# Kernel tuning notes

Hardware: AMD Instinct MI355X
Metric: run time of the kernel (lower is better)

## Reference

```python
import jax, jax.numpy as jnp
import numpy as np

IN_FEATURES = 4096
OUT_FEATURES = 11008


def setup_inputs() -> dict:
    key = jax.random.key(0)
    k1, k2, k3 = jax.random.split(key, 3)
    x = jax.random.normal(k1, (4, 2048, IN_FEATURES), dtype=jnp.float32)
    # int8-valued weights stored as int32 (range [-127, 127] emulated via [0,127) here)
    weight_quantized = jax.random.randint(k2, (OUT_FEATURES, IN_FEATURES), 0, 127, dtype=jnp.int32)
    weight_scale = jax.random.uniform(k3, (OUT_FEATURES,), dtype=jnp.float32) * 0.01 + 1e-4
    return {"x": x, "weight_quantized": weight_quantized, "weight_scale": weight_scale}


def reference(x, weight_quantized, weight_scale):
    # Dequantize: per-output-channel scale, then dense GEMM (F.linear semantics: y = x @ W^T)
    weight_fp = weight_quantized.astype(x.dtype) * weight_scale[:, None].astype(x.dtype)
    # x: [B, S, in], weight_fp: [out, in] -> [B, S, out]
    return jnp.einsum('bsi,oi->bso', x, weight_fp)
```

## Files before the change

### kernel.cpp

```cpp
#include <hip/hip_runtime.h>
#include <stdint.h>
#include <stddef.h>

#define M_DIM 8192
#define N_DIM 11008
#define K_DIM 4096

typedef __attribute__((ext_vector_type(8))) __bf16 bf16x8;
typedef __attribute__((ext_vector_type(4))) float f32x4;

typedef const __attribute__((address_space(1))) void gvoid;
typedef __attribute__((address_space(3))) void lvoid;

__device__ __forceinline__ void async16(const void* g, void* l) {
  __builtin_amdgcn_global_load_lds((gvoid*)g, (lvoid*)l, 16, 0, 0);
}

__device__ __forceinline__ unsigned short f2bf(float f) {
  unsigned u = __float_as_uint(f);
  u += 0x7fffu + ((u >> 16) & 1u);
  return (unsigned short)(u >> 16);
}


__global__ __launch_bounds__(256) void cvt_x_kernel(const float* __restrict__ x,
                                                    unsigned short* __restrict__ xw) {
  size_t i = ((size_t)blockIdx.x * 256 + threadIdx.x) * 4;
  float4 v = *(const float4*)(x + i);
  ushort4 o;
  o.x = f2bf(v.x); o.y = f2bf(v.y); o.z = f2bf(v.z); o.w = f2bf(v.w);
  *(ushort4*)(xw + i) = o;
}

__global__ __launch_bounds__(256) void cvt_w_kernel(const int* __restrict__ wq,
                                                    unsigned short* __restrict__ ww) {
  size_t i = ((size_t)blockIdx.x * 256 + threadIdx.x) * 4;
  int4 v = *(const int4*)(wq + i);
  ushort4 o;
  o.x = f2bf((float)v.x); o.y = f2bf((float)v.y);
  o.z = f2bf((float)v.z); o.w = f2bf((float)v.w);
  *(ushort4*)(ww + i) = o;
}


#define PH_MID                                            \
  __builtin_amdgcn_sched_barrier(0);                      \
  __builtin_amdgcn_s_barrier();                           \
  asm volatile("s_waitcnt lgkmcnt(0)" ::: "memory");      \
  __builtin_amdgcn_sched_barrier(0);                      \
  __builtin_amdgcn_s_setprio(1)

#define PH_END                                            \
  __builtin_amdgcn_s_setprio(0);                          \
  __builtin_amdgcn_sched_barrier(0);                      \
  __builtin_amdgcn_s_barrier()

#define PH_END_VM                                         \
  __builtin_amdgcn_s_setprio(0);                          \
  asm volatile("s_waitcnt vmcnt(4)" ::: "memory");        \
  __builtin_amdgcn_sched_barrier(0);                      \
  __builtin_amdgcn_s_barrier()

#define LD8(p, off) (*(const bf16x8*)((p) + (off)))

#define RD_A(PA0, PA1, IOFF)                                   \
  _Pragma("unroll") for (int ii = 0; ii < 4; ii++) {           \
    aR[ii][0] = LD8(PA0, ((IOFF) + ii) * 1024);                \
    aR[ii][1] = LD8(PA1, ((IOFF) + ii) * 1024);                \
  }

#define RD_B(BR, PB0, PB1, JOFF)                               \
  _Pragma("unroll") for (int jj = 0; jj < 2; jj++) {           \
    BR[jj][0] = LD8(PB0, ((JOFF) + jj) * 1024);                \
    BR[jj][1] = LD8(PB1, ((JOFF) + jj) * 1024);                \
  }

#define MFQ(IB, JB, BR)                                                         \
  _Pragma("unroll") for (int ii = 0; ii < 4; ii++)                              \
  _Pragma("unroll") for (int jj = 0; jj < 2; jj++)                              \
  _Pragma("unroll") for (int ss = 0; ss < 2; ss++)                              \
    acc[(IB) + ii][(JB) + jj] = __builtin_amdgcn_mfma_f32_16x16x32_bf16(        \
        aR[ii][ss], BR[jj][ss], acc[(IB) + ii][(JB) + jj], 0, 0, 0)

#define STG(g, s, h, u, kk)                                                     \
  async16((g) + (size_t)((h) * 128 + (u) * 64) * K_DIM + (kk),                  \
          (s) + ((h) * 128 + (u) * 64) * 64)

__global__ __launch_bounds__(512, 2) void gemm8(const unsigned short* __restrict__ xw,
                                                const unsigned short* __restrict__ ww,
                                                const float* __restrict__ scale,
                                                float* __restrict__ out) {
  extern __shared__ unsigned short smem[];

  const int tid = threadIdx.x;
  const int v = tid >> 6;
  const int l = tid & 63;
  const int wm = v >> 2, wn = v & 3;
  const int fm = l & 15, q = l >> 4;

  const int flat = blockIdx.x;
  const int swz = (flat & 7) * 172 + (flat >> 3);
  const int m0 = (swz & 31) * 256;
  const int n0 = (swz >> 5) * 256;

  const int sr = l >> 3;
  const int scn = (l & 7) ^ sr;
  const unsigned short* gA = xw + (size_t)(m0 + v * 8 + sr) * K_DIM + scn * 8;
  const unsigned short* gB = ww + (size_t)(n0 + v * 8 + sr) * K_DIM + scn * 8;
  unsigned short* const sA0 = smem + (v * 8) * 64;
  unsigned short* const sA1 = smem + 16384 + (v * 8) * 64;
  unsigned short* const sB0 = smem + 32768 + (v * 8) * 64;
  unsigned short* const sB1 = smem + 49152 + (v * 8) * 64;

  const int ca = q ^ (fm & 7);
  const unsigned short* const pA0 = smem + (wm * 128 + fm) * 64 + ca * 8;
  const unsigned short* const pA1 = smem + (wm * 128 + fm) * 64 + (ca ^ 4) * 8;
  const unsigned short* const pB0 = smem + 32768 + (wn * 64 + fm) * 64 + ca * 8;
  const unsigned short* const pB1 = smem + 32768 + (wn * 64 + fm) * 64 + (ca ^ 4) * 8;
  const unsigned short* const pA0o = pA0 + 16384;
  const unsigned short* const pA1o = pA1 + 16384;
  const unsigned short* const pB0o = pB0 + 16384;
  const unsigned short* const pB1o = pB1 + 16384;

  f32x4 acc[8][4];
#pragma unroll
  for (int i = 0; i < 8; i++)
#pragma unroll
    for (int j = 0; j < 4; j++) acc[i][j] = {0.f, 0.f, 0.f, 0.f};

  bf16x8 aR[4][2], b0R[2][2], b1R[2][2];

  STG(gA, sA0, 0, 0, 0); STG(gA, sA0, 0, 1, 0);
  STG(gA, sA0, 1, 0, 0); STG(gA, sA0, 1, 1, 0);
  STG(gB, sB0, 0, 0, 0); STG(gB, sB0, 0, 1, 0);
  STG(gB, sB0, 1, 0, 0); STG(gB, sB0, 1, 1, 0);
  STG(gA, sA1, 0, 0, 64); STG(gA, sA1, 0, 1, 64);
  STG(gA, sA1, 1, 0, 64); STG(gA, sA1, 1, 1, 64);
  asm volatile("s_waitcnt vmcnt(4)" ::: "memory");
  __builtin_amdgcn_sched_barrier(0);
  __builtin_amdgcn_s_barrier();

  for (int it2 = 0; it2 < K_DIM / 128; ++it2) {
    const int ka = it2 * 128;
    const int k1 = ka + 64;
    int k2 = ka + 128; if (k2 > K_DIM - 64) k2 = K_DIM - 64;
    int k3 = ka + 192; if (k3 > K_DIM - 64) k3 = K_DIM - 64;

    RD_A(pA0, pA1, 0);
    RD_B(b0R, pB0, pB1, 0);
    STG(gB, sB1, 0, 0, k1); STG(gB, sB1, 0, 1, k1);
    PH_MID; MFQ(0, 0, b0R); PH_END;

    RD_B(b1R, pB0, pB1, 2);
    STG(gB, sB1, 1, 0, k1); STG(gB, sB1, 1, 1, k1);
    PH_MID; MFQ(0, 2, b1R); PH_END;

    RD_A(pA0, pA1, 4);
    STG(gB, sB0, 0, 0, k2); STG(gB, sB0, 0, 1, k2);
    PH_MID; MFQ(4, 0, b0R); PH_END;

    STG(gA, sA0, 0, 0, k2); STG(gA, sA0, 0, 1, k2);
    PH_MID; MFQ(4, 2, b1R); PH_END_VM;

    RD_A(pA0o, pA1o, 0);
    RD_B(b0R, pB0o, pB1o, 0);
    STG(gA, sA0, 1, 0, k2); STG(gA, sA0, 1, 1, k2);
    PH_MID; MFQ(0, 0, b0R); PH_END;

    RD_B(b1R, pB0o, pB1o, 2);
    STG(gB, sB0, 1, 0, k2); STG(gB, sB0, 1, 1, k2);
    PH_MID; MFQ(0, 2, b1R); PH_END;

    RD_A(pA0o, pA1o, 4);
    __builtin_amdgcn_sched_barrier(0);
    STG(gA, sA1, 0, 0, k3); STG(gA, sA1, 0, 1, k3);
    PH_MID; MFQ(4, 0, b0R); PH_END;

    STG(gA, sA1, 1, 0, k3); STG(gA, sA1, 1, 1, k3);
    PH_MID; MFQ(4, 2, b1R); PH_END_VM;
  }

  float sc4[4];
  const int baseN = n0 + wn * 64 + fm;
#pragma unroll
  for (int j = 0; j < 4; j++) sc4[j] = scale[baseN + j * 16];
#pragma unroll
  for (int i = 0; i < 8; i++) {
#pragma unroll
    for (int r = 0; r < 4; r++) {
      size_t row = (size_t)(m0 + wm * 128 + i * 16 + q * 4 + r);
      float* po = out + row * N_DIM + baseN;
#pragma unroll
      for (int j = 0; j < 4; j++) po[j * 16] = acc[i][j][r] * sc4[j];
    }
  }
}


__global__ __launch_bounds__(256) void gemm_fused(const float* __restrict__ x,
                                                  const int* __restrict__ wq,
                                                  const float* __restrict__ scale,
                                                  float* __restrict__ out) {
  __shared__ unsigned short As[128 * 32];
  __shared__ unsigned short Bs[128 * 32];

  const int tid = threadIdx.x;
  const int w = tid >> 6, l = tid & 63;
  const int n0 = blockIdx.x * 128;
  const int m0 = blockIdx.y * 128;

  const int srow = tid >> 2;
  const int scol = (tid & 3) * 8;

  const int wm = w >> 1, wn = w & 1;
  const int fm = l & 15, q = l >> 4;
  const unsigned short* pA = &As[(wm * 64 + fm) * 32 + q * 8];
  const unsigned short* pB = &Bs[(wn * 64 + fm) * 32 + q * 8];

  f32x4 acc[4][4];
#pragma unroll
  for (int i = 0; i < 4; i++)
#pragma unroll
    for (int j = 0; j < 4; j++) acc[i][j] = {0.f, 0.f, 0.f, 0.f};

  for (int kk = 0; kk < K_DIM; kk += 32) {
    __syncthreads();
#pragma unroll
    for (int h = 0; h < 2; h++) {
      int row = h * 64 + srow;
      const float* pa = x + (size_t)(m0 + row) * K_DIM + kk + scol;
      float4 a0 = *(const float4*)pa;
      float4 a1 = *(const float4*)(pa + 4);
      union { unsigned short us[8]; bf16x8 vv; } ua;
      ua.us[0] = f2bf(a0.x); ua.us[1] = f2bf(a0.y); ua.us[2] = f2bf(a0.z); ua.us[3] = f2bf(a0.w);
      ua.us[4] = f2bf(a1.x); ua.us[5] = f2bf(a1.y); ua.us[6] = f2bf(a1.z); ua.us[7] = f2bf(a1.w);
      *(bf16x8*)&As[row * 32 + scol] = ua.vv;

      const int* pb = wq + (size_t)(n0 + row) * K_DIM + kk + scol;
      int4 b0 = *(const int4*)pb;
      int4 b1 = *(const int4*)(pb + 4);
      union { unsigned short us[8]; bf16x8 vv; } ub;
      ub.us[0] = f2bf((float)b0.x); ub.us[1] = f2bf((float)b0.y);
      ub.us[2] = f2bf((float)b0.z); ub.us[3] = f2bf((float)b0.w);
      ub.us[4] = f2bf((float)b1.x); ub.us[5] = f2bf((float)b1.y);
      ub.us[6] = f2bf((float)b1.z); ub.us[7] = f2bf((float)b1.w);
      *(bf16x8*)&Bs[row * 32 + scol] = ub.vv;
    }
    __syncthreads();

    bf16x8 af[4], bf[4];
#pragma unroll
    for (int i = 0; i < 4; i++) af[i] = *(const bf16x8*)(pA + i * 16 * 32);
#pragma unroll
    for (int j = 0; j < 4; j++) bf[j] = *(const bf16x8*)(pB + j * 16 * 32);
#pragma unroll
    for (int i = 0; i < 4; i++)
#pragma unroll
      for (int j = 0; j < 4; j++)
        acc[i][j] = __builtin_amdgcn_mfma_f32_16x16x32_bf16(af[i], bf[j], acc[i][j], 0, 0, 0);
  }

  float sc[4];
  const int baseN = n0 + wn * 64 + fm;
#pragma unroll
  for (int j = 0; j < 4; j++) sc[j] = scale[baseN + j * 16];
#pragma unroll
  for (int i = 0; i < 4; i++) {
#pragma unroll
    for (int r = 0; r < 4; r++) {
      size_t row = (size_t)(m0 + wm * 64 + i * 16 + q * 4 + r);
      float* po = out + row * N_DIM + baseN;
#pragma unroll
      for (int j = 0; j < 4; j++) po[j * 16] = acc[i][j][r] * sc[j];
    }
  }
}

extern "C" void kernel_launch(void* const* d_in, const int* in_sizes, int n_in,
                              void* d_out, int out_size, void* d_ws, size_t ws_size,
                              hipStream_t stream) {
  const float* x = (const float*)d_in[0];
  const int* wq = (const int*)d_in[1];
  const float* sc = (const float*)d_in[2];
  float* out = (float*)d_out;

  const size_t xE = (size_t)M_DIM * K_DIM;
  const size_t wE = (size_t)N_DIM * K_DIM;
  const size_t need = (xE + wE) * sizeof(unsigned short);

  if (ws_size >= need) {
    static bool attr_set = false;
    if (!attr_set) {
      (void)hipFuncSetAttribute(reinterpret_cast<const void*>(gemm8),
                                hipFuncAttributeMaxDynamicSharedMemorySize, 131072);
      attr_set = true;
    }
    unsigned short* xw = (unsigned short*)d_ws;
    unsigned short* ww = xw + xE;
    cvt_x_kernel<<<(unsigned)(xE / 1024), 256, 0, stream>>>(x, xw);
    cvt_w_kernel<<<(unsigned)(wE / 1024), 256, 0, stream>>>(wq, ww);
    gemm8<<<dim3((M_DIM / 256) * (N_DIM / 256)), dim3(512), 131072, stream>>>(xw, ww, sc, out);
  } else {
    gemm_fused<<<dim3(N_DIM / 128, M_DIM / 128), 256, 0, stream>>>(x, wq, sc, out);
  }
}
```

Baseline: 1.179 ms.

## Restructure GEMM inner loop to overlap LDS reads with MFMA and fuse converts

The main loop is reorganized so each phase issues a full 4x4 MFMA block over one K-half while prefetching the next A/B fragments from LDS into alternate register sets, with lgkmcnt waits moved to phase ends. This is meant to hide LDS read latency behind matrix instructions instead of stalling before each MFMA group. Separately, the two conversion kernels are merged into one grid-stride kernel that converts 8 elements per thread, removing a launch. The change raises register pressure (more fragment registers live) and alters the barrier/wait placement, which could hurt occupancy or ordering.

```diff
diff --git a/kernel.cpp b/kernel.cpp
--- a/kernel.cpp
+++ b/kernel.cpp
@@ -8,6 +8,7 @@
 
 typedef __attribute__((ext_vector_type(8))) __bf16 bf16x8;
 typedef __attribute__((ext_vector_type(4))) float f32x4;
+typedef __attribute__((ext_vector_type(8))) unsigned short u16x8;
 
 typedef const __attribute__((address_space(1))) void gvoid;
 typedef __attribute__((address_space(3))) void lvoid;
@@ -23,23 +24,29 @@
 }
 
 
-__global__ __launch_bounds__(256) void cvt_x_kernel(const float* __restrict__ x,
-                                                    unsigned short* __restrict__ xw) {
-  size_t i = ((size_t)blockIdx.x * 256 + threadIdx.x) * 4;
-  float4 v = *(const float4*)(x + i);
-  ushort4 o;
-  o.x = f2bf(v.x); o.y = f2bf(v.y); o.z = f2bf(v.z); o.w = f2bf(v.w);
-  *(ushort4*)(xw + i) = o;
-}
-
-__global__ __launch_bounds__(256) void cvt_w_kernel(const int* __restrict__ wq,
-                                                    unsigned short* __restrict__ ww) {
-  size_t i = ((size_t)blockIdx.x * 256 + threadIdx.x) * 4;
-  int4 v = *(const int4*)(wq + i);
-  ushort4 o;
-  o.x = f2bf((float)v.x); o.y = f2bf((float)v.y);
-  o.z = f2bf((float)v.z); o.w = f2bf((float)v.w);
-  *(ushort4*)(ww + i) = o;
+__global__ __launch_bounds__(256) void cvt_all(const float* __restrict__ x,
+                                               const int* __restrict__ wq,
+                                               unsigned short* __restrict__ xw,
+                                               unsigned short* __restrict__ ww) {
+  const size_t xc = (size_t)M_DIM * K_DIM / 8;
+  const size_t tc = xc + (size_t)N_DIM * K_DIM / 8;
+  for (size_t c = (size_t)blockIdx.x * 256 + threadIdx.x; c < tc;
+       c += (size_t)gridDim.x * 256) {
+    if (c < xc) {
+      const float4* p = (const float4*)(x + c * 8);
+      float4 a = p[0], b = p[1];
+      u16x8 o = {f2bf(a.x), f2bf(a.y), f2bf(a.z), f2bf(a.w),
+                 f2bf(b.x), f2bf(b.y), f2bf(b.z), f2bf(b.w)};
+      *(u16x8*)(xw + c * 8) = o;
+    } else {
+      const size_t d = c - xc;
+      const int4* p = (const int4*)(wq + d * 8);
+      int4 a = p[0], b = p[1];
+      u16x8 o = {f2bf((float)a.x), f2bf((float)a.y), f2bf((float)a.z), f2bf((float)a.w),
+                 f2bf((float)b.x), f2bf((float)b.y), f2bf((float)b.z), f2bf((float)b.w)};
+      *(u16x8*)(ww + d * 8) = o;
+    }
+  }
 }
 
 
@@ -52,35 +59,31 @@
 
 #define PH_END                                            \
   __builtin_amdgcn_s_setprio(0);                          \
+  asm volatile("s_waitcnt lgkmcnt(0)" ::: "memory");      \
   __builtin_amdgcn_sched_barrier(0);                      \
   __builtin_amdgcn_s_barrier()
 
 #define PH_END_VM                                         \
   __builtin_amdgcn_s_setprio(0);                          \
-  asm volatile("s_waitcnt vmcnt(4)" ::: "memory");        \
+  asm volatile("s_waitcnt vmcnt(4) lgkmcnt(0)" ::: "memory"); \
   __builtin_amdgcn_sched_barrier(0);                      \
   __builtin_amdgcn_s_barrier()
 
 #define LD8(p, off) (*(const bf16x8*)((p) + (off)))
 
-#define RD_A(PA0, PA1, IOFF)                                   \
-  _Pragma("unroll") for (int ii = 0; ii < 4; ii++) {           \
-    aR[ii][0] = LD8(PA0, ((IOFF) + ii) * 1024);                \
-    aR[ii][1] = LD8(PA1, ((IOFF) + ii) * 1024);                \
-  }
-
-#define RD_B(BR, PB0, PB1, JOFF)                               \
-  _Pragma("unroll") for (int jj = 0; jj < 2; jj++) {           \
-    BR[jj][0] = LD8(PB0, ((JOFF) + jj) * 1024);                \
-    BR[jj][1] = LD8(PB1, ((JOFF) + jj) * 1024);                \
-  }
-
-#define MFQ(IB, JB, BR)                                                         \
+#define RD_A4(DST, PBASE, MH)                                  \
+  _Pragma("unroll") for (int ii = 0; ii < 4; ii++)             \
+      DST[ii] = LD8(PBASE, ((MH) * 4 + ii) * 1024)
+
+#define RD_B4(DST, PBASE)                                      \
+  _Pragma("unroll") for (int jj = 0; jj < 4; jj++)             \
+      DST[jj] = LD8(PBASE, jj * 1024)
+
+#define MFQ16(MH, AR, BR)                                                       \
   _Pragma("unroll") for (int ii = 0; ii < 4; ii++)                              \
-  _Pragma("unroll") for (int jj = 0; jj < 2; jj++)                              \
-  _Pragma("unroll") for (int ss = 0; ss < 2; ss++)                              \
-    acc[(IB) + ii][(JB) + jj] = __builtin_amdgcn_mfma_f32_16x16x32_bf16(        \
-        aR[ii][ss], BR[jj][ss], acc[(IB) + ii][(JB) + jj], 0, 0, 0)
+  _Pragma("unroll") for (int jj = 0; jj < 4; jj++)                              \
+    acc[(MH) * 4 + ii][jj] = __builtin_amdgcn_mfma_f32_16x16x32_bf16(           \
+        AR[ii], BR[jj], acc[(MH) * 4 + ii][jj], 0, 0, 0)
 
 #define STG(g, s, h, u, kk)                                                     \
   async16((g) + (size_t)((h) * 128 + (u) * 64) * K_DIM + (kk),                  \
@@ -128,7 +131,7 @@
 #pragma unroll
     for (int j = 0; j < 4; j++) acc[i][j] = {0.f, 0.f, 0.f, 0.f};
 
-  bf16x8 aR[4][2], b0R[2][2], b1R[2][2];
+  bf16x8 aR0[4], aR1[4], bRA[4], bRB[4];
 
   STG(gA, sA0, 0, 0, 0); STG(gA, sA0, 0, 1, 0);
   STG(gA, sA0, 1, 0, 0); STG(gA, sA0, 1, 1, 0);
@@ -146,38 +149,58 @@
     int k2 = ka + 128; if (k2 > K_DIM - 64) k2 = K_DIM - 64;
     int k3 = ka + 192; if (k3 > K_DIM - 64) k3 = K_DIM - 64;
 
-    RD_A(pA0, pA1, 0);
-    RD_B(b0R, pB0, pB1, 0);
+    RD_A4(aR0, pA0, 0);
+    RD_B4(bRA, pB0);
     STG(gB, sB1, 0, 0, k1); STG(gB, sB1, 0, 1, k1);
-    PH_MID; MFQ(0, 0, b0R); PH_END;
-
-    RD_B(b1R, pB0, pB1, 2);
+    PH_MID;
+    MFQ16(0, aR0, bRA);
+    RD_A4(aR1, pA0, 1);
+    PH_END;
+
     STG(gB, sB1, 1, 0, k1); STG(gB, sB1, 1, 1, k1);
-    PH_MID; MFQ(0, 2, b1R); PH_END;
-
-    RD_A(pA0, pA1, 4);
+    PH_MID;
+    MFQ16(1, aR1, bRA);
+    RD_A4(aR0, pA1, 0);
+    RD_B4(bRB, pB1);
+    PH_END;
+
     STG(gB, sB0, 0, 0, k2); STG(gB, sB0, 0, 1, k2);
-    PH_MID; MFQ(4, 0, b0R); PH_END;
+    PH_MID;
+    MFQ16(0, aR0, bRB);
+    RD_A4(aR1, pA1, 1);
+    PH_END;
 
     STG(gA, sA0, 0, 0, k2); STG(gA, sA0, 0, 1, k2);
-    PH_MID; MFQ(4, 2, b1R); PH_END_VM;
-
-    RD_A(pA0o, pA1o, 0);
-    RD_B(b0R, pB0o, pB1o, 0);
+    PH_MID;
+    MFQ16(1, aR1, bRB);
+    PH_END_VM;
+
+    RD_A4(aR0, pA0o, 0);
+    RD_B4(bRA, pB0o);
     STG(gA, sA0, 1, 0, k2); STG(gA, sA0, 1, 1, k2);
-    PH_MID; MFQ(0, 0, b0R); PH_END;
-
-    RD_B(b1R, pB0o, pB1o, 2);
+    PH_MID;
+    MFQ16(0, aR0, bRA);
+    RD_A4(aR1, pA0o, 1);
+    PH_END;
+
     STG(gB, sB0, 1, 0, k2); STG(gB, sB0, 1, 1, k2);
-    PH_MID; MFQ(0, 2, b1R); PH_END;
-
-    RD_A(pA0o, pA1o, 4);
+    PH_MID;
+    MFQ16(1, aR1, bRA);
+    RD_A4(aR0, pA1o, 0);
+    RD_B4(bRB, pB1o);
+    PH_END;
+
+    RD_A4(aR1, pA1o, 1);
     __builtin_amdgcn_sched_barrier(0);
     STG(gA, sA1, 0, 0, k3); STG(gA, sA1, 0, 1, k3);
-    PH_MID; MFQ(4, 0, b0R); PH_END;
+    PH_MID;
+    MFQ16(0, aR0, bRB);
+    PH_END;
 
     STG(gA, sA1, 1, 0, k3); STG(gA, sA1, 1, 1, k3);
-    PH_MID; MFQ(4, 2, b1R); PH_END_VM;
+    PH_MID;
+    MFQ16(1, aR1, bRB);
+    PH_END_VM;
   }
 
   float sc4[4];
@@ -297,8 +320,7 @@
     }
     unsigned short* xw = (unsigned short*)d_ws;
     unsigned short* ww = xw + xE;
-    cvt_x_kernel<<<(unsigned)(xE / 1024), 256, 0, stream>>>(x, xw);
-    cvt_w_kernel<<<(unsigned)(wE / 1024), 256, 0, stream>>>(wq, ww);
+    cvt_all<<<2048, 256, 0, stream>>>(x, wq, xw, ww);
     gemm8<<<dim3((M_DIM / 256) * (N_DIM / 256)), dim3(512), 131072, stream>>>(xw, ww, sc, out);
   } else {
     gemm_fused<<<dim3(N_DIM / 128, M_DIM / 128), 256, 0, stream>>>(x, wq, sc, out);
```

After: 1.195 ms. Within noise of the previous version (+1.4%).
